# Kernel tuning notes

Hardware: AMD Instinct MI355X
Metric: run time of the kernel (lower is better)

The kernel has to match this reference:

```python
import jax, jax.numpy as jnp
import numpy as np

HEAD_DIM = 64
SCALE = HEAD_DIM ** -0.5
NUM_HEADS = 16


def setup_inputs() -> dict:
    key = jax.random.key(0)
    k1, k2, k3, k4 = jax.random.split(key, 4)
    dim = 1024
    query = jax.random.normal(k1, (8, 512, dim), dtype=jnp.float32)
    memory = jax.random.normal(k2, (8, 512, dim), dtype=jnp.float32)
    # nn.Linear weights are [out, in]; scale like default init
    W_Q = jax.random.normal(k3, (dim, dim), dtype=jnp.float32) * (dim ** -0.5)
    W_K = jax.random.normal(k4, (dim, dim), dtype=jnp.float32) * (dim ** -0.5)
    return {"query": query, "memory": memory, "W_Q": W_Q, "W_K": W_K}


def reference(query, memory, W_Q, W_K):
    # Q: [K, Lq, E], K: [B, Lk, E]  (E = H * D)
    Q = query @ W_Q.T
    Km = memory @ W_K.T
    Kb, Lq, E = Q.shape
    Bb, Lk, _ = Km.shape
    Qh = Q.reshape(Kb, Lq, NUM_HEADS, HEAD_DIM).transpose(0, 2, 1, 3)  # K H q D
    Kh = Km.reshape(Bb, Lk, NUM_HEADS, HEAD_DIM).transpose(0, 2, 1, 3)  # B H k D
    # logits: [B, K, H, q, k]
    logits = jnp.einsum('ahqd,bhkd->bahqk', Qh, Kh) * SCALE
    energies = jax.nn.logsumexp(logits, axis=-2) / SCALE  # [B, K, H, k]
    energies = energies.mean(axis=1)  # [B, H, k]
    return energies
```

## Files before the change

kernel.cpp:

```cpp
#include <hip/hip_runtime.h>
#include <hip/hip_bf16.h>

typedef short short8 __attribute__((ext_vector_type(8)));
typedef float f32x4 __attribute__((ext_vector_type(4)));
typedef unsigned short u16;

__device__ __forceinline__ unsigned short f2bf(float f) {
  unsigned int u = __float_as_uint(f);
  u += 0x7fffu + ((u >> 16) & 1u);
  return (unsigned short)(u >> 16);
}

__device__ __forceinline__ void glds16(const void* g, void* l) {
  __builtin_amdgcn_global_load_lds(
      (const __attribute__((address_space(1))) unsigned int*)g,
      (__attribute__((address_space(3))) unsigned int*)l, 16, 0, 0);
}

__device__ __forceinline__ void drain_then_sync() {
  __builtin_amdgcn_s_waitcnt(0);
  __syncthreads();
}

__global__ __launch_bounds__(256) void prep(const float4* __restrict__ q,
                                            const float4* __restrict__ m,
                                            const float4* __restrict__ wq,
                                            const float4* __restrict__ wk,
                                            ushort4* __restrict__ qb,
                                            ushort4* __restrict__ mb,
                                            ushort4* __restrict__ wqb,
                                            ushort4* __restrict__ wkb,
                                            float4* __restrict__ out0) {
  const int i = blockIdx.x * 256 + threadIdx.x;
  const float c = 0.18033688011112042f;
  if (i < 1048576) {
    float4 v = q[i];
    ushort4 o; o.x = f2bf(v.x); o.y = f2bf(v.y); o.z = f2bf(v.z); o.w = f2bf(v.w);
    qb[i] = o;
  } else if (i < 2097152) {
    float4 v = m[i - 1048576];
    ushort4 o; o.x = f2bf(v.x); o.y = f2bf(v.y); o.z = f2bf(v.z); o.w = f2bf(v.w);
    mb[i - 1048576] = o;
  } else if (i < 2359296) {
    float4 v = wq[i - 2097152];
    ushort4 o; o.x = f2bf(v.x * c); o.y = f2bf(v.y * c); o.z = f2bf(v.z * c); o.w = f2bf(v.w * c);
    wqb[i - 2097152] = o;
  } else if (i < 2621440) {
    float4 v = wk[i - 2359296];
    ushort4 o; o.x = f2bf(v.x); o.y = f2bf(v.y); o.z = f2bf(v.z); o.w = f2bf(v.w);
    wkb[i - 2359296] = o;
  } else if (i < 2637824) {
    out0[i - 2621440] = (float4){0.f, 0.f, 0.f, 0.f};
  }
}

__global__ __launch_bounds__(512) void gemm_db(const u16* __restrict__ A0,
                                               const u16* __restrict__ B0,
                                               u16* __restrict__ C0,
                                               const u16* __restrict__ A1,
                                               const u16* __restrict__ B1,
                                               u16* __restrict__ C1) {
  __shared__ u16 As[2][128 * 64];
  __shared__ u16 Bs[2][128 * 64];
  const int zz = blockIdx.x & 1;
  const u16* A = zz ? A1 : A0;
  const u16* B = zz ? B1 : B0;
  u16* C = zz ? C1 : C0;
  const int t = threadIdx.x;
  const int lane = t & 63, wave = t >> 6;
  const int l15 = lane & 15, quad = lane >> 4;
  const int mb = (blockIdx.x >> 1) * 128;
  const int nb = blockIdx.y * 128;
  const int wm = (wave & 1) * 64;
  const int wn = (wave >> 1) * 32;

  const int srow = lane >> 3;
  const int scol = ((lane & 7) ^ srow) * 8;
  const int sw = l15 & 7;

  f32x4 acc[4][2];
#pragma unroll
  for (int i = 0; i < 4; i++)
#pragma unroll
    for (int j = 0; j < 2; j++) acc[i][j] = (f32x4){0.f, 0.f, 0.f, 0.f};

#pragma unroll
  for (int j = 0; j < 2; j++) {
    const int g = wave * 2 + j;
    glds16(A + (size_t)(mb + g * 8 + srow) * 1024 + scol, &As[0][g * 512 + lane * 8]);
    glds16(B + (size_t)(nb + g * 8 + srow) * 1024 + scol, &Bs[0][g * 512 + lane * 8]);
  }

  for (int it = 0; it < 16; ++it) {
    drain_then_sync();
    if (it < 15) {
      const int kb = (it + 1) * 64, bf_ = (it + 1) & 1;
#pragma unroll
      for (int j = 0; j < 2; j++) {
        const int g = wave * 2 + j;
        glds16(A + (size_t)(mb + g * 8 + srow) * 1024 + kb + scol, &As[bf_][g * 512 + lane * 8]);
        glds16(B + (size_t)(nb + g * 8 + srow) * 1024 + kb + scol, &Bs[bf_][g * 512 + lane * 8]);
      }
    }
    const u16* as = As[it & 1];
    const u16* bs = Bs[it & 1];
#pragma unroll
    for (int kk = 0; kk < 2; kk++) {
      const int cb = kk * 4;
      short8 af[4], bfr[2];
#pragma unroll
      for (int mi = 0; mi < 4; mi++)
        af[mi] = *(const short8*)&as[(wm + mi * 16 + l15) * 64 + ((cb + quad) ^ sw) * 8];
#pragma unroll
      for (int ni = 0; ni < 2; ni++)
        bfr[ni] = *(const short8*)&bs[(wn + ni * 16 + l15) * 64 + ((cb + quad) ^ sw) * 8];
#pragma unroll
      for (int mi = 0; mi < 4; mi++)
#pragma unroll
        for (int ni = 0; ni < 2; ni++)
          acc[mi][ni] = __builtin_amdgcn_mfma_f32_16x16x32_bf16(
              af[mi], bfr[ni], acc[mi][ni], 0, 0, 0);
    }
  }

#pragma unroll
  for (int mi = 0; mi < 4; mi++)
#pragma unroll
    for (int r = 0; r < 4; r++) {
      const int row = mb + wm + mi * 16 + quad * 4 + r;
      const size_t base = (size_t)row * 1024 + nb + wn;
#pragma unroll
      for (int ni = 0; ni < 2; ni++)
        C[base + ni * 16 + l15] = f2bf(acc[mi][ni][r]);
    }
}

__global__ __launch_bounds__(256) void attn_lse2(const u16* __restrict__ Qp,
                                                 const u16* __restrict__ Kp,
                                                 float* __restrict__ out) {
  __shared__ u16 qs[256 * 64];
  const int t = threadIdx.x;
  const int lane = t & 63, wave = t >> 6;
  const int l15 = lane & 15, quad = lane >> 4;
  const int kt = blockIdx.x & 1, aa = blockIdx.x >> 1;
  const int h = blockIdx.y, b = blockIdx.z;
  const int kwave = kt * 256 + wave * 64;

  short8 klo[4], khi[4];
#pragma unroll
  for (int tt = 0; tt < 4; tt++) {
    const short8* kg = (const short8*)(Kp + (size_t)(b * 512 + kwave + tt * 16 + l15) * 1024
                                       + h * 64 + quad * 8);
    klo[tt] = kg[0];
    khi[tt] = kg[4];
  }

  const int srow = lane >> 3;
  const int scol = ((lane & 7) ^ srow) * 8;
  const u16* qbase = Qp + (size_t)(aa * 512) * 1024 + h * 64;

  const int sw = l15 & 7;
  const int colLo = (quad ^ sw) * 8;
  const int colHi = ((4 + quad) ^ sw) * 8;
  const int rrow = l15 * 64;

  f32x4 csv0 = (f32x4){0.f, 0.f, 0.f, 0.f};
  f32x4 csv1 = csv0, csv2 = csv0, csv3 = csv0;

  for (int s = 0; s < 2; ++s) {
    if (s) __syncthreads();
#pragma unroll
    for (int j = 0; j < 8; ++j) {
      const int g = wave * 8 + j;
      glds16(qbase + (size_t)(s * 256 + g * 8 + srow) * 1024 + scol,
             &qs[g * 512 + lane * 8]);
    }
    drain_then_sync();

    for (int ii = 0; ii < 4; ++ii) {
      const u16* buf = qs + ii * 4096;
#pragma unroll
      for (int qt = 0; qt < 4; ++qt) {
        short8 alo = *(const short8*)&buf[qt * 1024 + rrow + colLo];
        short8 ahi = *(const short8*)&buf[qt * 1024 + rrow + colHi];
        f32x4 ac0 = (f32x4){0.f, 0.f, 0.f, 0.f};
        f32x4 ac1 = ac0, ac2 = ac0, ac3 = ac0;
        ac0 = __builtin_amdgcn_mfma_f32_16x16x32_bf16(alo, klo[0], ac0, 0, 0, 0);
        ac0 = __builtin_amdgcn_mfma_f32_16x16x32_bf16(ahi, khi[0], ac0, 0, 0, 0);
        ac1 = __builtin_amdgcn_mfma_f32_16x16x32_bf16(alo, klo[1], ac1, 0, 0, 0);
        ac1 = __builtin_amdgcn_mfma_f32_16x16x32_bf16(ahi, khi[1], ac1, 0, 0, 0);
        ac2 = __builtin_amdgcn_mfma_f32_16x16x32_bf16(alo, klo[2], ac2, 0, 0, 0);
        ac2 = __builtin_amdgcn_mfma_f32_16x16x32_bf16(ahi, khi[2], ac2, 0, 0, 0);
        ac3 = __builtin_amdgcn_mfma_f32_16x16x32_bf16(alo, klo[3], ac3, 0, 0, 0);
        ac3 = __builtin_amdgcn_mfma_f32_16x16x32_bf16(ahi, khi[3], ac3, 0, 0, 0);
#pragma unroll
        for (int r = 0; r < 4; r++) {
          csv0[r] += __builtin_amdgcn_exp2f(ac0[r]);
          csv1[r] += __builtin_amdgcn_exp2f(ac1[r]);
          csv2[r] += __builtin_amdgcn_exp2f(ac2[r]);
          csv3[r] += __builtin_amdgcn_exp2f(ac3[r]);
        }
      }
    }
  }
  float cs0 = csv0[0] + csv0[1] + csv0[2] + csv0[3];
  float cs1 = csv1[0] + csv1[1] + csv1[2] + csv1[3];
  float cs2 = csv2[0] + csv2[1] + csv2[2] + csv2[3];
  float cs3 = csv3[0] + csv3[1] + csv3[2] + csv3[3];
  cs0 += __shfl_xor(cs0, 16); cs0 += __shfl_xor(cs0, 32);
  cs1 += __shfl_xor(cs1, 16); cs1 += __shfl_xor(cs1, 32);
  cs2 += __shfl_xor(cs2, 16); cs2 += __shfl_xor(cs2, 32);
  cs3 += __shfl_xor(cs3, 16); cs3 += __shfl_xor(cs3, 32);
  const float v = quad == 0 ? cs0 : quad == 1 ? cs1 : quad == 2 ? cs2 : cs3;
  atomicAdd(out + (size_t)b * 8192 + h * 512 + kwave + quad * 16 + l15, __logf(v));
}

extern "C" void kernel_launch(void* const* d_in, const int* in_sizes, int n_in,
                              void* d_out, int out_size, void* d_ws, size_t ws_size,
                              hipStream_t stream) {
  const float* query  = (const float*)d_in[0];
  const float* memory = (const float*)d_in[1];
  const float* wq     = (const float*)d_in[2];
  const float* wk     = (const float*)d_in[3];
  float* out = (float*)d_out;

  char* ws = (char*)d_ws;
  const size_t MB = 1024 * 1024;
  u16* qb  = (u16*)(ws);
  u16* mb_ = (u16*)(ws + 8  * MB);
  u16* wqb = (u16*)(ws + 16 * MB);
  u16* wkb = (u16*)(ws + 18 * MB);
  u16* Qp  = (u16*)(ws + 20 * MB);
  u16* Kp  = (u16*)(ws + 28 * MB);

  prep<<<10304, 256, 0, stream>>>((const float4*)query, (const float4*)memory,
                                  (const float4*)wq, (const float4*)wk,
                                  (ushort4*)qb, (ushort4*)mb_, (ushort4*)wqb,
                                  (ushort4*)wkb, (float4*)d_out);
  gemm_db<<<dim3(64, 8), 512, 0, stream>>>(qb, wqb, Qp, mb_, wkb, Kp);
  attn_lse2<<<dim3(16, 16, 8), 256, 0, stream>>>(Qp, Kp, out);
}
```

Baseline: 165.7 us.

## Double-buffer per-wave Q staging in attention kernel to overlap loads with MFMA

Each wave now streams all 512 query rows through its own pair of 32-row LDS buffers instead of sharing a 256-row block buffer between two barrier-synced phases. The next chunk's global-to-LDS loads are issued before computing on the current one, and a vmcnt wait replaces the block-wide drain and __syncthreads. This is meant to hide global load latency and remove block barriers. Each wave now loads the full Q tile on its own, so Q traffic is repeated per wave (likely served from cache), and the number of waits goes up.

```diff
diff --git a/kernel.cpp b/kernel.cpp
--- a/kernel.cpp
+++ b/kernel.cpp
@@ -135,10 +135,10 @@
     }
 }
 
-__global__ __launch_bounds__(256) void attn_lse2(const u16* __restrict__ Qp,
+__global__ __launch_bounds__(256) void attn_lse3(const u16* __restrict__ Qp,
                                                  const u16* __restrict__ Kp,
                                                  float* __restrict__ out) {
-  __shared__ u16 qs[256 * 64];
+  __shared__ u16 qs[4][2][32 * 64];
   const int t = threadIdx.x;
   const int lane = t & 63, wave = t >> 6;
   const int l15 = lane & 15, quad = lane >> 4;
@@ -157,49 +157,57 @@
 
   const int srow = lane >> 3;
   const int scol = ((lane & 7) ^ srow) * 8;
-  const u16* qbase = Qp + (size_t)(aa * 512) * 1024 + h * 64;
+  const u16* qc = Qp + (size_t)(aa * 512 + srow) * 1024 + h * 64 + scol;
 
   const int sw = l15 & 7;
   const int colLo = (quad ^ sw) * 8;
   const int colHi = ((4 + quad) ^ sw) * 8;
   const int rrow = l15 * 64;
 
+  u16* const buf0 = &qs[wave][0][0];
+  u16* const buf1 = &qs[wave][1][0];
+  const int ldst = lane * 8;
+
   f32x4 csv0 = (f32x4){0.f, 0.f, 0.f, 0.f};
   f32x4 csv1 = csv0, csv2 = csv0, csv3 = csv0;
 
-  for (int s = 0; s < 2; ++s) {
-    if (s) __syncthreads();
-#pragma unroll
-    for (int j = 0; j < 8; ++j) {
-      const int g = wave * 8 + j;
-      glds16(qbase + (size_t)(s * 256 + g * 8 + srow) * 1024 + scol,
-             &qs[g * 512 + lane * 8]);
-    }
-    drain_then_sync();
-
-    for (int ii = 0; ii < 4; ++ii) {
-      const u16* buf = qs + ii * 4096;
-#pragma unroll
-      for (int qt = 0; qt < 4; ++qt) {
-        short8 alo = *(const short8*)&buf[qt * 1024 + rrow + colLo];
-        short8 ahi = *(const short8*)&buf[qt * 1024 + rrow + colHi];
-        f32x4 ac0 = (f32x4){0.f, 0.f, 0.f, 0.f};
-        f32x4 ac1 = ac0, ac2 = ac0, ac3 = ac0;
-        ac0 = __builtin_amdgcn_mfma_f32_16x16x32_bf16(alo, klo[0], ac0, 0, 0, 0);
-        ac0 = __builtin_amdgcn_mfma_f32_16x16x32_bf16(ahi, khi[0], ac0, 0, 0, 0);
-        ac1 = __builtin_amdgcn_mfma_f32_16x16x32_bf16(alo, klo[1], ac1, 0, 0, 0);
-        ac1 = __builtin_amdgcn_mfma_f32_16x16x32_bf16(ahi, khi[1], ac1, 0, 0, 0);
-        ac2 = __builtin_amdgcn_mfma_f32_16x16x32_bf16(alo, klo[2], ac2, 0, 0, 0);
-        ac2 = __builtin_amdgcn_mfma_f32_16x16x32_bf16(ahi, khi[2], ac2, 0, 0, 0);
-        ac3 = __builtin_amdgcn_mfma_f32_16x16x32_bf16(alo, klo[3], ac3, 0, 0, 0);
-        ac3 = __builtin_amdgcn_mfma_f32_16x16x32_bf16(ahi, khi[3], ac3, 0, 0, 0);
-#pragma unroll
-        for (int r = 0; r < 4; r++) {
-          csv0[r] += __builtin_amdgcn_exp2f(ac0[r]);
-          csv1[r] += __builtin_amdgcn_exp2f(ac1[r]);
-          csv2[r] += __builtin_amdgcn_exp2f(ac2[r]);
-          csv3[r] += __builtin_amdgcn_exp2f(ac3[r]);
-        }
+#pragma unroll
+  for (int g = 0; g < 4; ++g)
+    glds16(qc + (size_t)g * 8 * 1024, buf0 + g * 512 + ldst);
+
+  for (int c = 0; c < 16; ++c) {
+    const u16* cur = (c & 1) ? buf1 : buf0;
+    u16* nxt = (c & 1) ? buf0 : buf1;
+    if (c < 15) {
+      const u16* qn = qc + (size_t)(c + 1) * 32 * 1024;
+#pragma unroll
+      for (int g = 0; g < 4; ++g)
+        glds16(qn + (size_t)g * 8 * 1024, nxt + g * 512 + ldst);
+      asm volatile("s_waitcnt vmcnt(4)" ::: "memory");
+    } else {
+      asm volatile("s_waitcnt vmcnt(0)" ::: "memory");
+    }
+    __builtin_amdgcn_sched_barrier(0);
+#pragma unroll
+    for (int qt = 0; qt < 2; ++qt) {
+      short8 alo = *(const short8*)&cur[qt * 1024 + rrow + colLo];
+      short8 ahi = *(const short8*)&cur[qt * 1024 + rrow + colHi];
+      f32x4 ac0 = (f32x4){0.f, 0.f, 0.f, 0.f};
+      f32x4 ac1 = ac0, ac2 = ac0, ac3 = ac0;
+      ac0 = __builtin_amdgcn_mfma_f32_16x16x32_bf16(alo, klo[0], ac0, 0, 0, 0);
+      ac0 = __builtin_amdgcn_mfma_f32_16x16x32_bf16(ahi, khi[0], ac0, 0, 0, 0);
+      ac1 = __builtin_amdgcn_mfma_f32_16x16x32_bf16(alo, klo[1], ac1, 0, 0, 0);
+      ac1 = __builtin_amdgcn_mfma_f32_16x16x32_bf16(ahi, khi[1], ac1, 0, 0, 0);
+      ac2 = __builtin_amdgcn_mfma_f32_16x16x32_bf16(alo, klo[2], ac2, 0, 0, 0);
+      ac2 = __builtin_amdgcn_mfma_f32_16x16x32_bf16(ahi, khi[2], ac2, 0, 0, 0);
+      ac3 = __builtin_amdgcn_mfma_f32_16x16x32_bf16(alo, klo[3], ac3, 0, 0, 0);
+      ac3 = __builtin_amdgcn_mfma_f32_16x16x32_bf16(ahi, khi[3], ac3, 0, 0, 0);
+#pragma unroll
+      for (int r = 0; r < 4; r++) {
+        csv0[r] += __builtin_amdgcn_exp2f(ac0[r]);
+        csv1[r] += __builtin_amdgcn_exp2f(ac1[r]);
+        csv2[r] += __builtin_amdgcn_exp2f(ac2[r]);
+        csv3[r] += __builtin_amdgcn_exp2f(ac3[r]);
       }
     }
   }
@@ -238,5 +246,5 @@
                                   (ushort4*)qb, (ushort4*)mb_, (ushort4*)wqb,
                                   (ushort4*)wkb, (float4*)d_out);
   gemm_db<<<dim3(64, 8), 512, 0, stream>>>(qb, wqb, Qp, mb_, wkb, Kp);
-  attn_lse2<<<dim3(16, 16, 8), 256, 0, stream>>>(Qp, Kp, out);
-}
+  attn_lse3<<<dim3(16, 16, 8), 256, 0, stream>>>(Qp, Kp, out);
+}
```

After: 151.8 us. 1.09x faster.
